# Optimization experiments

Hardware: AMD Instinct MI355X
Metric: run time of the kernel (lower is better)

## Reference

```python
import jax, jax.numpy as jnp
import numpy as np

B, N, F_IN, F_OUT = 8, 2048, 128, 64
ALPHA = 0.2  # LeakyReLU negative slope
NEG_INF = -9e15


def setup_inputs() -> dict:
    key = jax.random.key(0)
    k1, k2, k3, k4 = jax.random.split(key, 4)
    h = jax.random.normal(k1, (B, N, F_IN), dtype=jnp.float32)
    adj = jax.random.randint(k2, (B, N, N), 0, 2, dtype=jnp.int32)
    # xavier_uniform with gain=1.414 approximated by scaled normals (values are arbitrary params)
    W = jax.random.normal(k3, (F_IN, F_OUT), dtype=jnp.float32) * (1.414 * np.sqrt(2.0 / (F_IN + F_OUT)))
    a = jax.random.normal(k4, (2 * F_OUT, 1), dtype=jnp.float32) * (1.414 * np.sqrt(2.0 / (2 * F_OUT + 1)))
    return {"h": h, "adj": adj, "W": W, "a": a}


def reference(h, adj, W, a):
    # Wh: [B, N, F_out]
    Wh = jnp.einsum('bnf,fo->bno', h, W)
    Fo = W.shape[1]
    a1 = a[:Fo, 0]   # [F_out]
    a2 = a[Fo:, 0]   # [F_out]
    # e[b,i,j] = leakyrelu(Wh[b,i]@a1 + Wh[b,j]@a2)  (== cat(Wh_i,Wh_j)@a, same math, no N^2*2F blowup)
    e1 = jnp.einsum('bno,o->bn', Wh, a1)  # [B, N]
    e2 = jnp.einsum('bno,o->bn', Wh, a2)  # [B, N]
    e = e1[:, :, None] + e2[:, None, :]   # [B, N, N]
    e = jnp.where(e > 0, e, ALPHA * e)    # LeakyReLU
    e = jnp.where(adj > 0, e, NEG_INF)    # mask non-edges
    attention = jax.nn.softmax(e, axis=-1)
    # dropout is identity in inference mode (deterministic reference)
    h_prime = jnp.einsum('bij,bjo->bio', attention, Wh)  # [B, N, F_out]
    return jax.nn.elu(h_prime)  # concat=True branch
```

## Files before the change

kernel.cpp:

```cpp
#include <hip/hip_runtime.h>
#include <hip/hip_bf16.h>

#define BB 8
#define NN 2048
#define FIN 128
#define FO 64
#define ALPHA 0.2f

typedef __attribute__((ext_vector_type(8))) short bf16x8;
typedef __attribute__((ext_vector_type(4))) float f32x4;
typedef __attribute__((ext_vector_type(4))) int i32x4;

typedef __attribute__((address_space(1))) const void gvoid;
typedef __attribute__((address_space(3))) void lvoid;

__device__ inline void gl_lds16(const void* g, void* l) {
    __builtin_amdgcn_global_load_lds((gvoid*)g, (lvoid*)l, 16, 0, 0);
}

__device__ inline short f2bf(float x) {
    unsigned u = __float_as_uint(x);
    u += 0x7fffu + ((u >> 16) & 1u);
    return (short)(u >> 16);
}

__global__ __launch_bounds__(256) void wh_kernel(
    const float* __restrict__ h, const float* __restrict__ W,
    const float* __restrict__ a, float* __restrict__ e1, float* __restrict__ e2,
    float* __restrict__ e2p, short* __restrict__ whF)
{
    const int t  = threadIdx.x;
    const int o  = t & 63;
    const int wv = t >> 6;
    const int r0 = blockIdx.x * 32;
    const float* __restrict__ hrow =
        h + (size_t)(r0 + __builtin_amdgcn_readfirstlane(wv) * 8) * FIN;

    float acc[8];
#pragma unroll
    for (int rr = 0; rr < 8; rr++) acc[rr] = 0.f;

    for (int f = 0; f < FIN; f += 4) {
        const float w0 = W[(f + 0) * FO + o];
        const float w1 = W[(f + 1) * FO + o];
        const float w2 = W[(f + 2) * FO + o];
        const float w3 = W[(f + 3) * FO + o];
#pragma unroll
        for (int rr = 0; rr < 8; rr++) {
            const float4 hv = *(const float4*)(hrow + rr * FIN + f);
            acc[rr] = fmaf(hv.x, w0, acc[rr]);
            acc[rr] = fmaf(hv.y, w1, acc[rr]);
            acc[rr] = fmaf(hv.z, w2, acc[rr]);
            acc[rr] = fmaf(hv.w, w3, acc[rr]);
        }
    }

    const int b   = r0 / NN;
    const int ib0 = r0 - b * NN;
    const int ibb = ib0 + wv * 8;
    const int jc  = ibb >> 5;
    const int qq  = (ibb >> 3) & 3;
    const int ot  = o >> 4, mm = o & 15;
    const int L   = mm + qq * 16;
    bf16x8 frag;
#pragma unroll
    for (int rr = 0; rr < 8; rr++) frag[rr] = f2bf(acc[rr]);
    *(bf16x8*)(whF + ((((size_t)(b * 64 + jc) * 4 + ot) * 64 + L) * 8)) = frag;

    const float a1 = a[o], a2 = a[FO + o];
    float vmax = -3.0e38f;
#pragma unroll
    for (int rr = 0; rr < 8; rr++) {
        float v1 = acc[rr] * a1, v2 = acc[rr] * a2;
#pragma unroll
        for (int msk = 32; msk >= 1; msk >>= 1) {
            v1 += __shfl_xor(v1, msk, 64);
            v2 += __shfl_xor(v2, msk, 64);
        }
        vmax = fmaxf(vmax, v2);
        if (o == 0) { e1[r0 + wv * 8 + rr] = v1; e2[r0 + wv * 8 + rr] = v2; }
    }
    if (o == 0) e2p[b * 256 + (ib0 >> 5) * 4 + wv] = vmax;
}

struct SMemS { int adj[16][516]; float e2[512]; };
struct SMemC { float comb[4][16][64]; float lsum[4][16]; };
union __align__(16) SMemU { SMemS s; SMemC c; };

__global__ __launch_bounds__(256, 4) void attn_kernel(
    const int* __restrict__ adj, const float* __restrict__ e1,
    const float* __restrict__ e2, const float* __restrict__ e2p,
    const short* __restrict__ whF, float* __restrict__ out)
{
    __shared__ SMemU sm;
    __shared__ float red4[4];
    const int t = threadIdx.x, w = t >> 6, lane = t & 63;
    const int m = lane & 15, q = lane >> 4;
    const int blk = blockIdx.x;
    const int b  = blk >> 7;
    const int i0 = (blk & 127) * 16;
    const int i  = i0 + m;

    float pv = e2p[b * 256 + t];
    const float e1v = e1[b * NN + i];
#pragma unroll
    for (int k = 32; k >= 1; k >>= 1) pv = fmaxf(pv, __shfl_xor(pv, k, 64));
    if (lane == 0) red4[w] = pv;
    __syncthreads();
    const float e2mx = fmaxf(fmaxf(red4[0], red4[1]), fmaxf(red4[2], red4[3]));

    float mi = e1v + e2mx;
    mi = mi > 0.f ? mi : ALPHA * mi;

    const short* whFb = whF + (size_t)b * (64 * 4 * 64 * 8);
    const int* arow = adj + (size_t)(b * NN + i0 + w * 4) * NN + lane * 4;
    const float* e2g = e2 + b * NN + lane * 4;

    f32x4 acc0 = {0.f,0.f,0.f,0.f}, acc1 = acc0, acc2 = acc0, acc3 = acc0;
    float lsum = 0.f;

    for (int tt = 0; tt < 4; tt++) {
        const int j0 = tt * 512;
#pragma unroll
        for (int rr = 0; rr < 4; rr++) {
            const int* src = arow + (size_t)rr * NN + j0;
            gl_lds16(src,        &sm.s.adj[w * 4 + rr][0]);
            gl_lds16(src + 256,  &sm.s.adj[w * 4 + rr][256]);
        }
        if (w == 0) {
            gl_lds16(e2g + j0,        &sm.s.e2[0]);
            gl_lds16(e2g + j0 + 256,  &sm.s.e2[256]);
        }
        __syncthreads();

#pragma unroll
        for (int s2 = 0; s2 < 4; s2++) {
            const int col = w * 128 + s2 * 32 + q * 8;
            i32x4 a0 = *(const i32x4*)&sm.s.adj[m][col];
            i32x4 a1 = *(const i32x4*)&sm.s.adj[m][col + 4];
            f32x4 ev0 = *(const f32x4*)&sm.s.e2[col];
            f32x4 ev1 = *(const f32x4*)&sm.s.e2[col + 4];

            bf16x8 af;
#pragma unroll
            for (int jj = 0; jj < 8; jj++) {
                const int   av  = (jj < 4) ? a0[jj]      : a1[jj - 4];
                const float e2j = (jj < 4) ? ev0[jj]     : ev1[jj - 4];
                float e = e1v + e2j;
                e = e > 0.f ? e : ALPHA * e;
                const float pe = (av > 0) ? __expf(e - mi) : 0.f;
                lsum += pe;
                af[jj] = f2bf(pe);
            }

            const int jc = (j0 + w * 128 + s2 * 32) >> 5;
            const short* bfp = whFb + (size_t)jc * 2048 + lane * 8;
            bf16x8 b0 = *(const bf16x8*)(bfp);
            bf16x8 b1 = *(const bf16x8*)(bfp + 512);
            bf16x8 b2 = *(const bf16x8*)(bfp + 1024);
            bf16x8 b3 = *(const bf16x8*)(bfp + 1536);

            acc0 = __builtin_amdgcn_mfma_f32_16x16x32_bf16(af, b0, acc0, 0, 0, 0);
            acc1 = __builtin_amdgcn_mfma_f32_16x16x32_bf16(af, b1, acc1, 0, 0, 0);
            acc2 = __builtin_amdgcn_mfma_f32_16x16x32_bf16(af, b2, acc2, 0, 0, 0);
            acc3 = __builtin_amdgcn_mfma_f32_16x16x32_bf16(af, b3, acc3, 0, 0, 0);
        }
        __syncthreads();
    }

    lsum += __shfl_xor(lsum, 16, 64);
    lsum += __shfl_xor(lsum, 32, 64);
    if (q == 0) sm.c.lsum[w][m] = lsum;
#pragma unroll
    for (int ot = 0; ot < 4; ot++) {
        f32x4 av = (ot == 0) ? acc0 : (ot == 1) ? acc1 : (ot == 2) ? acc2 : acc3;
#pragma unroll
        for (int reg = 0; reg < 4; reg++)
            sm.c.comb[w][q * 4 + reg][ot * 16 + m] = av[reg];
    }
    __syncthreads();

    const int row = t >> 4, c0 = (t & 15) * 4;
    f32x4 sum = *(const f32x4*)&sm.c.comb[0][row][c0];
#pragma unroll
    for (int ww = 1; ww < 4; ww++) {
        f32x4 sv = *(const f32x4*)&sm.c.comb[ww][row][c0];
        sum.x += sv.x; sum.y += sv.y; sum.z += sv.z; sum.w += sv.w;
    }
    float l = sm.c.lsum[0][row] + sm.c.lsum[1][row] + sm.c.lsum[2][row] + sm.c.lsum[3][row];
    l = fmaxf(l, 1e-30f);
    const float rl = 1.f / l;
    float vr[4] = { sum.x * rl, sum.y * rl, sum.z * rl, sum.w * rl };
    f32x4 res;
#pragma unroll
    for (int kk = 0; kk < 4; kk++)
        res[kk] = vr[kk] > 0.f ? vr[kk] : (__expf(vr[kk]) - 1.f);
    *(f32x4*)&out[((size_t)(b * NN + i0 + row)) * FO + c0] = res;
}

extern "C" void kernel_launch(void* const* d_in, const int* in_sizes, int n_in,
                              void* d_out, int out_size, void* d_ws, size_t ws_size,
                              hipStream_t stream) {
    const float* h   = (const float*)d_in[0];
    const int*   adj = (const int*)d_in[1];
    const float* W   = (const float*)d_in[2];
    const float* a   = (const float*)d_in[3];
    float* out = (float*)d_out;

    char* ws = (char*)d_ws;
    short* whF = (short*)ws;
    size_t off = (size_t)BB * 64 * 4 * 64 * 8 * sizeof(short);
    float* e1  = (float*)(ws + off);  off += (size_t)BB * NN * 4;
    float* e2  = (float*)(ws + off);  off += (size_t)BB * NN * 4;
    float* e2p = (float*)(ws + off);

    wh_kernel<<<(BB * NN) / 32, 256, 0, stream>>>(h, W, a, e1, e2, e2p, whF);
    attn_kernel<<<BB * (NN / 16), 256, 0, stream>>>(adj, e1, e2, e2p, whF, out);
}
```

Measured before the change: 224.8 us.

## Pre-pack adjacency into bitmasks and read bits directly in attention kernel

Adds a pack kernel that converts the int32 adjacency matrix into 64-bit ballot bitmasks. The attention kernel then reads these compact bits straight from global memory instead of staging int32 adjacency tiles through LDS. This removes the LDS round trip and the per-tile barriers, and shrinks the traffic in the compute kernel. In exchange it adds an extra kernel launch and a workspace buffer, and the full adjacency matrix is still read once.

```diff
diff --git a/kernel.cpp b/kernel.cpp
--- a/kernel.cpp
+++ b/kernel.cpp
@@ -10,18 +10,34 @@
 typedef __attribute__((ext_vector_type(8))) short bf16x8;
 typedef __attribute__((ext_vector_type(4))) float f32x4;
 typedef __attribute__((ext_vector_type(4))) int i32x4;
-
-typedef __attribute__((address_space(1))) const void gvoid;
-typedef __attribute__((address_space(3))) void lvoid;
-
-__device__ inline void gl_lds16(const void* g, void* l) {
-    __builtin_amdgcn_global_load_lds((gvoid*)g, (lvoid*)l, 16, 0, 0);
-}
+typedef __attribute__((ext_vector_type(2))) unsigned long long u64x2;
 
 __device__ inline short f2bf(float x) {
     unsigned u = __float_as_uint(x);
     u += 0x7fffu + ((u >> 16) & 1u);
     return (short)(u >> 16);
+}
+
+__global__ __launch_bounds__(256) void pack_kernel(
+    const int* __restrict__ adj, unsigned long long* __restrict__ ab)
+{
+    const int lane = threadIdx.x & 63;
+    const int wid  = (blockIdx.x << 2) + (threadIdx.x >> 6);
+    const int* src = adj + (size_t)wid * (32 * 256) + lane * 4;
+#pragma unroll 4
+    for (int c = 0; c < 32; c++) {
+        i32x4 v = *(const i32x4*)(src + c * 256);
+        unsigned long long b0 = __ballot(v[0] > 0);
+        unsigned long long b1 = __ballot(v[1] > 0);
+        unsigned long long b2 = __ballot(v[2] > 0);
+        unsigned long long b3 = __ballot(v[3] > 0);
+        if (lane == 0) {
+            u64x2* d = (u64x2*)(ab + ((size_t)wid * 32 + c) * 4);
+            u64x2 lo; lo[0] = b0; lo[1] = b1;
+            u64x2 hi; hi[0] = b2; hi[1] = b3;
+            d[0] = lo; d[1] = hi;
+        }
+    }
 }
 
 __global__ __launch_bounds__(256) void wh_kernel(
@@ -83,17 +99,14 @@
     if (o == 0) e2p[b * 256 + (ib0 >> 5) * 4 + wv] = vmax;
 }
 
-struct SMemS { int adj[16][516]; float e2[512]; };
-struct SMemC { float comb[4][16][64]; float lsum[4][16]; };
-union __align__(16) SMemU { SMemS s; SMemC c; };
-
-__global__ __launch_bounds__(256, 4) void attn_kernel(
-    const int* __restrict__ adj, const float* __restrict__ e1,
+struct SMemC { float comb[4][16][64]; float lsum[4][16]; float red4[4]; };
+
+__global__ __launch_bounds__(256) void attn_kernel(
+    const unsigned long long* __restrict__ ab, const float* __restrict__ e1,
     const float* __restrict__ e2, const float* __restrict__ e2p,
     const short* __restrict__ whF, float* __restrict__ out)
 {
-    __shared__ SMemU sm;
-    __shared__ float red4[4];
+    __shared__ SMemC sm;
     const int t = threadIdx.x, w = t >> 6, lane = t & 63;
     const int m = lane & 15, q = lane >> 4;
     const int blk = blockIdx.x;
@@ -105,89 +118,85 @@
     const float e1v = e1[b * NN + i];
 #pragma unroll
     for (int k = 32; k >= 1; k >>= 1) pv = fmaxf(pv, __shfl_xor(pv, k, 64));
-    if (lane == 0) red4[w] = pv;
+    if (lane == 0) sm.red4[w] = pv;
     __syncthreads();
-    const float e2mx = fmaxf(fmaxf(red4[0], red4[1]), fmaxf(red4[2], red4[3]));
+    const float e2mx = fmaxf(fmaxf(sm.red4[0], sm.red4[1]),
+                             fmaxf(sm.red4[2], sm.red4[3]));
 
     float mi = e1v + e2mx;
     mi = mi > 0.f ? mi : ALPHA * mi;
 
     const short* whFb = whF + (size_t)b * (64 * 4 * 64 * 8);
-    const int* arow = adj + (size_t)(b * NN + i0 + w * 4) * NN + lane * 4;
-    const float* e2g = e2 + b * NN + lane * 4;
+    const float* e2b = e2 + b * NN;
+    const unsigned long long* abrow = ab + (size_t)(b * NN + i) * 32;
 
     f32x4 acc0 = {0.f,0.f,0.f,0.f}, acc1 = acc0, acc2 = acc0, acc3 = acc0;
     float lsum = 0.f;
 
-    for (int tt = 0; tt < 4; tt++) {
-        const int j0 = tt * 512;
-#pragma unroll
-        for (int rr = 0; rr < 4; rr++) {
-            const int* src = arow + (size_t)rr * NN + j0;
-            gl_lds16(src,        &sm.s.adj[w * 4 + rr][0]);
-            gl_lds16(src + 256,  &sm.s.adj[w * 4 + rr][256]);
-        }
-        if (w == 0) {
-            gl_lds16(e2g + j0,        &sm.s.e2[0]);
-            gl_lds16(e2g + j0 + 256,  &sm.s.e2[256]);
-        }
-        __syncthreads();
-
-#pragma unroll
-        for (int s2 = 0; s2 < 4; s2++) {
-            const int col = w * 128 + s2 * 32 + q * 8;
-            i32x4 a0 = *(const i32x4*)&sm.s.adj[m][col];
-            i32x4 a1 = *(const i32x4*)&sm.s.adj[m][col + 4];
-            f32x4 ev0 = *(const f32x4*)&sm.s.e2[col];
-            f32x4 ev1 = *(const f32x4*)&sm.s.e2[col + 4];
-
-            bf16x8 af;
-#pragma unroll
-            for (int jj = 0; jj < 8; jj++) {
-                const int   av  = (jj < 4) ? a0[jj]      : a1[jj - 4];
-                const float e2j = (jj < 4) ? ev0[jj]     : ev1[jj - 4];
-                float e = e1v + e2j;
-                e = e > 0.f ? e : ALPHA * e;
-                const float pe = (av > 0) ? __expf(e - mi) : 0.f;
-                lsum += pe;
-                af[jj] = f2bf(pe);
-            }
-
-            const int jc = (j0 + w * 128 + s2 * 32) >> 5;
+#pragma unroll
+    for (int tt = 0; tt < 8; tt++) {
+        u64x2 Ba = *(const u64x2*)(abrow + tt * 4);
+        u64x2 Bb = *(const u64x2*)(abrow + tt * 4 + 2);
+        const unsigned long long B0 = Ba[0], B1 = Ba[1], B2 = Bb[0], B3 = Bb[1];
+
+#pragma unroll
+        for (int s2 = 0; s2 < 2; s2++) {
+            const int col = w * 64 + s2 * 32 + q * 8;
+            const int sh = col >> 2;
+            const unsigned long long C0 = B0 >> sh, C1 = B1 >> sh,
+                                     C2 = B2 >> sh, C3 = B3 >> sh;
+
+            f32x4 ev0 = *(const f32x4*)(e2b + tt * 256 + col);
+            f32x4 ev1 = *(const f32x4*)(e2b + tt * 256 + col + 4);
+
+            const int jc = tt * 8 + w * 2 + s2;
             const short* bfp = whFb + (size_t)jc * 2048 + lane * 8;
             bf16x8 b0 = *(const bf16x8*)(bfp);
             bf16x8 b1 = *(const bf16x8*)(bfp + 512);
             bf16x8 b2 = *(const bf16x8*)(bfp + 1024);
             bf16x8 b3 = *(const bf16x8*)(bfp + 1536);
 
+            bf16x8 af;
+#pragma unroll
+            for (int jj = 0; jj < 8; jj++) {
+                const unsigned long long Cw =
+                    (jj & 3) == 0 ? C0 : (jj & 3) == 1 ? C1 : (jj & 3) == 2 ? C2 : C3;
+                const bool av = (Cw >> (jj >> 2)) & 1ull;
+                const float e2j = (jj < 4) ? ev0[jj] : ev1[jj - 4];
+                float e = e1v + e2j;
+                e = e > 0.f ? e : ALPHA * e;
+                const float pe = av ? __expf(e - mi) : 0.f;
+                lsum += pe;
+                af[jj] = f2bf(pe);
+            }
+
             acc0 = __builtin_amdgcn_mfma_f32_16x16x32_bf16(af, b0, acc0, 0, 0, 0);
             acc1 = __builtin_amdgcn_mfma_f32_16x16x32_bf16(af, b1, acc1, 0, 0, 0);
             acc2 = __builtin_amdgcn_mfma_f32_16x16x32_bf16(af, b2, acc2, 0, 0, 0);
             acc3 = __builtin_amdgcn_mfma_f32_16x16x32_bf16(af, b3, acc3, 0, 0, 0);
         }
-        __syncthreads();
     }
 
     lsum += __shfl_xor(lsum, 16, 64);
     lsum += __shfl_xor(lsum, 32, 64);
-    if (q == 0) sm.c.lsum[w][m] = lsum;
+    if (q == 0) sm.lsum[w][m] = lsum;
 #pragma unroll
     for (int ot = 0; ot < 4; ot++) {
         f32x4 av = (ot == 0) ? acc0 : (ot == 1) ? acc1 : (ot == 2) ? acc2 : acc3;
 #pragma unroll
         for (int reg = 0; reg < 4; reg++)
-            sm.c.comb[w][q * 4 + reg][ot * 16 + m] = av[reg];
+            sm.comb[w][q * 4 + reg][ot * 16 + m] = av[reg];
     }
     __syncthreads();
 
     const int row = t >> 4, c0 = (t & 15) * 4;
-    f32x4 sum = *(const f32x4*)&sm.c.comb[0][row][c0];
+    f32x4 sum = *(const f32x4*)&sm.comb[0][row][c0];
 #pragma unroll
     for (int ww = 1; ww < 4; ww++) {
-        f32x4 sv = *(const f32x4*)&sm.c.comb[ww][row][c0];
+        f32x4 sv = *(const f32x4*)&sm.comb[ww][row][c0];
         sum.x += sv.x; sum.y += sv.y; sum.z += sv.z; sum.w += sv.w;
     }
-    float l = sm.c.lsum[0][row] + sm.c.lsum[1][row] + sm.c.lsum[2][row] + sm.c.lsum[3][row];
+    float l = sm.lsum[0][row] + sm.lsum[1][row] + sm.lsum[2][row] + sm.lsum[3][row];
     l = fmaxf(l, 1e-30f);
     const float rl = 1.f / l;
     float vr[4] = { sum.x * rl, sum.y * rl, sum.z * rl, sum.w * rl };
@@ -212,8 +221,10 @@
     size_t off = (size_t)BB * 64 * 4 * 64 * 8 * sizeof(short);
     float* e1  = (float*)(ws + off);  off += (size_t)BB * NN * 4;
     float* e2  = (float*)(ws + off);  off += (size_t)BB * NN * 4;
-    float* e2p = (float*)(ws + off);
-
+    float* e2p = (float*)(ws + off);  off += (size_t)BB * 256 * 4;
+    unsigned long long* adjbits = (unsigned long long*)(ws + off);
+
+    pack_kernel<<<1024, 256, 0, stream>>>(adj, adjbits);
     wh_kernel<<<(BB * NN) / 32, 256, 0, stream>>>(h, W, a, e1, e2, e2p, whF);
-    attn_kernel<<<BB * (NN / 16), 256, 0, stream>>>(adj, e1, e2, e2p, whF, out);
-}
+    attn_kernel<<<BB * (NN / 16), 256, 0, stream>>>(adjbits, e1, e2, e2p, whF, out);
+}
```

After: 250.7 us. +11.5%, slower.
